# Performance work log

Hardware: AMD Instinct MI355X
Metric: run time of the kernel (lower is better)

The kernel has to match this reference:

```python
import jax, jax.numpy as jnp
import numpy as np

NUM_GRAPHS = 512  # number of segments (graphs) in the batch
N_NODES = 200000
HIDDEN = 256


def setup_inputs() -> dict:
    key = jax.random.key(0)
    ks = jax.random.split(key, 8)
    x = jax.random.normal(ks[0], (N_NODES, HIDDEN), dtype=jnp.float32)
    batch = jnp.sort(jax.random.randint(ks[1], (N_NODES,), 0, NUM_GRAPHS, dtype=jnp.int32))
    h4 = HIDDEN // 4
    w1 = jax.random.normal(ks[2], (HIDDEN, h4), dtype=jnp.float32) * (1.0 / np.sqrt(HIDDEN))
    b1 = jnp.zeros((h4,), dtype=jnp.float32)
    w2 = jax.random.normal(ks[3], (h4, 1), dtype=jnp.float32) * (1.0 / np.sqrt(h4))
    b2 = jnp.zeros((1,), dtype=jnp.float32)
    wp = jax.random.normal(ks[4], (3 * HIDDEN, HIDDEN), dtype=jnp.float32) * (1.0 / np.sqrt(3 * HIDDEN))
    bp = jnp.zeros((HIDDEN,), dtype=jnp.float32)
    gamma = jnp.ones((HIDDEN,), dtype=jnp.float32)
    beta = jnp.zeros((HIDDEN,), dtype=jnp.float32)
    return {"x": x, "batch": batch, "w1": w1, "b1": b1, "w2": w2, "b2": b2,
            "wp": wp, "bp": bp, "gamma": gamma, "beta": beta}


def reference(x, batch, w1, b1, w2, b2, wp, bp, gamma, beta):
    G = NUM_GRAPHS
    # --- global mean pool ---
    seg_sum = jax.ops.segment_sum(x, batch, num_segments=G)  # [G, H]
    counts = jax.ops.segment_sum(jnp.ones((x.shape[0],), x.dtype), batch, num_segments=G)
    z_mean = seg_sum / jnp.maximum(counts, 1.0)[:, None]
    # --- global max pool ---
    z_max = jax.ops.segment_max(x, batch, num_segments=G)
    z_max = jnp.where(jnp.isfinite(z_max), z_max, 0.0)  # guard empty segments
    # --- global attention pool (PyG GlobalAttention) ---
    gate = jnp.maximum(x @ w1 + b1, 0.0) @ w2 + b2  # [N, 1]
    g = gate[:, 0]
    g_max = jax.ops.segment_max(g, batch, num_segments=G)
    g_max = jnp.where(jnp.isfinite(g_max), g_max, 0.0)
    e = jnp.exp(g - g_max[batch])
    denom = jax.ops.segment_sum(e, batch, num_segments=G)
    w = e / jnp.maximum(denom, 1e-16)[batch]  # scatter-softmax weights [N]
    z_attn = jax.ops.segment_sum(w[:, None] * x, batch, num_segments=G)
    # --- concat + proj + layernorm ---
    z = jnp.concatenate([z_mean, z_max, z_attn], axis=-1)  # [G, 3H]
    y = z @ wp + bp  # [G, H]
    mu = jnp.mean(y, axis=-1, keepdims=True)
    var = jnp.mean(jnp.square(y - mu), axis=-1, keepdims=True)
    yhat = (y - mu) * jax.lax.rsqrt(var + 1e-5)
    return yhat * gamma + beta
```

## Files before the change

kernel.cpp:

```cpp
#include <hip/hip_runtime.h>
#include <math.h>

#define N_NODES 200000
#define NGRAPH  512
#define HID     256
#define NTILES  (N_NODES / 16)
#define NBLK    256
#define NWAVE   (NBLK * 4)
#define TPW     (NTILES / NWAVE)
#define TREM    (NTILES - NWAVE * TPW)

typedef __attribute__((ext_vector_type(8))) short s16x8;
typedef __attribute__((ext_vector_type(4))) float f32x4;

__device__ __forceinline__ unsigned int pack2_bf16_rne(float a, float b) {
  unsigned int ua = __float_as_uint(a), ub = __float_as_uint(b);
  unsigned int ra = (ua + 0x7fffu + ((ua >> 16) & 1u)) >> 16;
  unsigned int rb = (ub + 0x7fffu + ((ub >> 16) & 1u)) & 0xffff0000u;
  return ra | rb;
}
__device__ __forceinline__ int lower_bound_batch(const int* __restrict__ batch, int target) {
  int lo = 0, hi = N_NODES;
  while (lo < hi) { int mid = (lo + hi) >> 1; if (batch[mid] < target) lo = mid + 1; else hi = mid; }
  return lo;
}
__device__ __forceinline__ unsigned fkey(float f) {
  unsigned u = __float_as_uint(f);
  return (u >> 31) ? ~u : (u | 0x80000000u);
}

__global__ __launch_bounds__(256, 1) void fused_gate_pool(
    const float* __restrict__ x, const int* __restrict__ batch,
    const float* __restrict__ w1, const float* __restrict__ b1,
    const float* __restrict__ w2, const float* __restrict__ b2,
    float* __restrict__ gsum, unsigned* __restrict__ gmx,
    float* __restrict__ gat, float* __restrict__ gden)
{
  struct Buf { float xrow[16][256]; int bat[64]; };
  __shared__ __align__(16) Buf stg[4][2];

  const int tid = threadIdx.x;
  const int w = tid >> 6, lane = tid & 63, q = lane >> 4, c = lane & 15;
  const int gw = blockIdx.x * 4 + w;

  const int t0   = gw * TPW + (gw < TREM ? gw : TREM);
  const int tend = t0 + TPW + (gw < TREM ? 1 : 0);

  s16x8 bh[4][8];
#pragma unroll
  for (int nt = 0; nt < 4; ++nt) {
#pragma unroll
    for (int kt = 0; kt < 8; ++kt) {
      float f[8];
#pragma unroll
      for (int j = 0; j < 8; ++j)
        f[j] = w1[(size_t)(kt * 32 + q * 8 + j) * 64 + nt * 16 + c];
      union { s16x8 v; unsigned u[4]; } tmp;
      tmp.u[0] = pack2_bf16_rne(f[0], f[1]);
      tmp.u[1] = pack2_bf16_rne(f[2], f[3]);
      tmp.u[2] = pack2_bf16_rne(f[4], f[5]);
      tmp.u[3] = pack2_bf16_rne(f[6], f[7]);
      bh[nt][kt] = tmp.v;
    }
  }
  float b1v[4], w2v[4];
#pragma unroll
  for (int nt = 0; nt < 4; ++nt) { b1v[nt] = b1[nt * 16 + c]; w2v[nt] = w2[nt * 16 + c]; }
  const float b2v = b2[0];

  int soff[8];
#pragma unroll
  for (int s = 0; s < 8; ++s) soff[s] = (lane * 16) ^ (s << 4);
  const int csw = (c & 7) << 4;

  f32x4 sum = (f32x4){0.f, 0.f, 0.f, 0.f};
  f32x4 at  = (f32x4){0.f, 0.f, 0.f, 0.f};
  f32x4 mx  = (f32x4){-INFINITY, -INFINITY, -INFINITY, -INFINITY};
  float den = 0.f;
  int curseg = -1;

  auto STAGE = [&](int t, int b) {
    const char* rowbase = (const char*)x + (size_t)t * 16384;
#pragma unroll
    for (int r = 0; r < 16; ++r) {
      const void* gp = rowbase + r * 1024 + soff[r & 7];
      __builtin_amdgcn_global_load_lds(
          (const __attribute__((address_space(1))) void*)gp,
          (__attribute__((address_space(3))) void*)&stg[w][b].xrow[r][0],
          16, 0, 0);
    }
    const void* bp2 = (const void*)(batch + t * 16 + (lane & 15));
    __builtin_amdgcn_global_load_lds(
        (const __attribute__((address_space(1))) void*)bp2,
        (__attribute__((address_space(3))) void*)&stg[w][b].bat[0],
        4, 0, 0);
  };

  auto FLUSH = [&](int seg) {
    float* sp = gsum + (size_t)seg * 256 + lane * 4;
    float* ap = gat  + (size_t)seg * 256 + lane * 4;
    unsigned* mp = gmx + (size_t)seg * 256 + lane * 4;
#pragma unroll
    for (int j = 0; j < 4; ++j) {
      atomicAdd(&sp[j], sum[j]);
      atomicAdd(&ap[j], at[j]);
      atomicMax(&mp[j], fkey(mx[j]));
    }
    if (lane == 0) atomicAdd(&gden[seg], den);
  };

  STAGE(t0, 0);
  STAGE(t0 + 1, 1);

  for (int t = t0; t < tend; ++t) {
    const int b = (t - t0) & 1;
    if (t + 1 < tend) { asm volatile("s_waitcnt vmcnt(17)" ::: "memory"); }
    else              { asm volatile("s_waitcnt vmcnt(0)"  ::: "memory"); }
    __builtin_amdgcn_sched_barrier(0);

    const char* rb = (const char*)&stg[w][b].xrow[c][0];
    union { s16x8 v; unsigned u[4]; } ah[8];
#pragma unroll
    for (int kt = 0; kt < 8; ++kt) {
      const int base = kt * 128 + q * 32;
      float4 t0v = *(const float4*)(rb + ((base)      ^ csw));
      float4 t1v = *(const float4*)(rb + ((base + 16) ^ csw));
      ah[kt].u[0] = pack2_bf16_rne(t0v.x, t0v.y);
      ah[kt].u[1] = pack2_bf16_rne(t0v.z, t0v.w);
      ah[kt].u[2] = pack2_bf16_rne(t1v.x, t1v.y);
      ah[kt].u[3] = pack2_bf16_rne(t1v.z, t1v.w);
    }

    f32x4 acc[4];
#pragma unroll
    for (int nt = 0; nt < 4; ++nt) acc[nt] = (f32x4){0.f, 0.f, 0.f, 0.f};
#pragma unroll
    for (int kt = 0; kt < 8; ++kt) {
#pragma unroll
      for (int nt = 0; nt < 4; ++nt)
        acc[nt] = __builtin_amdgcn_mfma_f32_16x16x32_bf16(ah[kt].v, bh[nt][kt], acc[nt], 0, 0, 0);
    }

    float er[4];
#pragma unroll
    for (int r = 0; r < 4; ++r) {
      float sv = 0.f;
#pragma unroll
      for (int nt = 0; nt < 4; ++nt) {
        float h = acc[nt][r] + b1v[nt];
        h = h > 0.f ? h : 0.f;
        sv += h * w2v[nt];
      }
      sv += __shfl_xor(sv, 1, 64);
      sv += __shfl_xor(sv, 2, 64);
      sv += __shfl_xor(sv, 4, 64);
      sv += __shfl_xor(sv, 8, 64);
      er[r] = __expf(sv + b2v);
    }

#pragma unroll
    for (int i = 0; i < 16; ++i) {
      int sg = __builtin_amdgcn_readfirstlane(stg[w][b].bat[i]);
      if (sg != curseg) {
        if (curseg >= 0) FLUSH(curseg);
        sum = (f32x4){0.f, 0.f, 0.f, 0.f};
        at  = (f32x4){0.f, 0.f, 0.f, 0.f};
        mx  = (f32x4){-INFINITY, -INFINITY, -INFINITY, -INFINITY};
        den = 0.f;
        curseg = sg;
      }
      float ei = __shfl(er[i & 3], (i >> 2) << 4, 64);
      const float4 v = *(const float4*)((const char*)&stg[w][b].xrow[i][0] +
                                        ((lane * 16) ^ ((i & 7) << 4)));
      den += ei;
      sum[0] += v.x; sum[1] += v.y; sum[2] += v.z; sum[3] += v.w;
      mx[0] = fmaxf(mx[0], v.x); mx[1] = fmaxf(mx[1], v.y);
      mx[2] = fmaxf(mx[2], v.z); mx[3] = fmaxf(mx[3], v.w);
      at[0] = fmaf(ei, v.x, at[0]); at[1] = fmaf(ei, v.y, at[1]);
      at[2] = fmaf(ei, v.z, at[2]); at[3] = fmaf(ei, v.w, at[3]);
    }

    if (t + 2 < tend) STAGE(t + 2, b);
  }
  if (curseg >= 0) FLUSH(curseg);
}

__global__ __launch_bounds__(256) void head_ln(
    const float* __restrict__ gsum, const unsigned* __restrict__ gmx,
    const float* __restrict__ gat, const float* __restrict__ gden,
    const int* __restrict__ batch, const float* __restrict__ wp,
    const float* __restrict__ bp, const float* __restrict__ gam,
    const float* __restrict__ bet, float* __restrict__ out)
{
  const int g = blockIdx.x;
  const int tid = threadIdx.x;
  const int w = tid >> 6, lane = tid & 63;
  __shared__ int sb[2];
  __shared__ float z[768];
  __shared__ __align__(16) float part[4][256];
  __shared__ float red[256];

  if (tid < 2) sb[tid] = lower_bound_batch(batch, g + tid);
  __syncthreads();
  const float cnt = (float)(sb[1] - sb[0]);

  {
    const float s = gsum[(size_t)g * 256 + tid];
    const unsigned k = gmx[(size_t)g * 256 + tid];
    const unsigned u = (k & 0x80000000u) ? (k ^ 0x80000000u) : ~k;
    const float a = gat[(size_t)g * 256 + tid];
    const float den = gden[g];
    z[tid]       = (cnt > 0.f) ? s / cnt : 0.f;
    z[256 + tid] = (cnt > 0.f) ? __uint_as_float(u) : 0.f;
    z[512 + tid] = a / fmaxf(den, 1e-16f);
  }
  __syncthreads();

  f32x4 acc = (f32x4){0.f, 0.f, 0.f, 0.f};
  const float4* wp4 = (const float4*)wp;
  const int k0 = w * 192;
#pragma unroll 8
  for (int k = k0; k < k0 + 192; ++k) {
    float4 wv = wp4[(size_t)k * 64 + lane];
    float zk = z[k];
    acc[0] = fmaf(zk, wv.x, acc[0]);
    acc[1] = fmaf(zk, wv.y, acc[1]);
    acc[2] = fmaf(zk, wv.z, acc[2]);
    acc[3] = fmaf(zk, wv.w, acc[3]);
  }
  *(f32x4*)&part[w][lane * 4] = acc;
  __syncthreads();

  const int t = tid;
  float y = bp[t] + part[0][t] + part[1][t] + part[2][t] + part[3][t];

  red[t] = y;
  __syncthreads();
  for (int wd = 128; wd > 0; wd >>= 1) {
    if (t < wd) red[t] += red[t + wd];
    __syncthreads();
  }
  const float mu = red[0] * (1.f / 256.f);
  __syncthreads();
  float d = y - mu;
  red[t] = d * d;
  __syncthreads();
  for (int wd = 128; wd > 0; wd >>= 1) {
    if (t < wd) red[t] += red[t + wd];
    __syncthreads();
  }
  const float var = red[0] * (1.f / 256.f);
  const float is = rsqrtf(var + 1e-5f);
  out[(size_t)g * 256 + t] = fmaf(d * is, gam[t], bet[t]);
}

extern "C" void kernel_launch(void* const* d_in, const int* in_sizes, int n_in,
                              void* d_out, int out_size, void* d_ws, size_t ws_size,
                              hipStream_t stream) {
  const float* x   = (const float*)d_in[0];
  const int*   bat = (const int*)d_in[1];
  const float* w1  = (const float*)d_in[2];
  const float* b1  = (const float*)d_in[3];
  const float* w2  = (const float*)d_in[4];
  const float* b2  = (const float*)d_in[5];
  const float* wp  = (const float*)d_in[6];
  const float* bp  = (const float*)d_in[7];
  const float* gam = (const float*)d_in[8];
  const float* bet = (const float*)d_in[9];
  float* out = (float*)d_out;

  float* gsum   = (float*)d_ws;
  unsigned* gmx = (unsigned*)(gsum + (size_t)NGRAPH * 256);
  float* gat    = (float*)(gmx + (size_t)NGRAPH * 256);
  float* gden   = gat + (size_t)NGRAPH * 256;
  const size_t zbytes = ((size_t)NGRAPH * 256 * 3 + NGRAPH) * 4;

  hipMemsetAsync(d_ws, 0, zbytes, stream);
  hipLaunchKernelGGL(fused_gate_pool, dim3(NBLK), dim3(256), 0, stream,
                     x, bat, w1, b1, w2, b2, gsum, gmx, gat, gden);
  hipLaunchKernelGGL(head_ln, dim3(NGRAPH), dim3(256), 0, stream,
                     gsum, gmx, gat, gden, bat, wp, bp, gam, bet, out);
}
```

Before: 339.7 us.

## Replace LDS-direct double buffering with register prefetch and two blocks per CU

Drops the global_load_lds double-buffered staging and instead prefetches the next 16-row tile into registers, writing it into a single swizzled LDS buffer each iteration. It doubles the grid to 512 blocks with launch bounds allowing 2 blocks per CU, relying on occupancy rather than explicit vmcnt pipelining to hide latency. It also reads segment ids from global memory and adds a fast path when a whole tile belongs to one segment. This costs extra VGPRs for the prefetch and puts scalar batch loads on the critical path. With one LDS buffer, the wave's own reads and writes must stay ordered.

Result: slower. 462.9 us (+36.2%).

```diff
diff --git a/kernel.cpp b/kernel.cpp
--- a/kernel.cpp
+++ b/kernel.cpp
@@ -5,7 +5,7 @@
 #define NGRAPH  512
 #define HID     256
 #define NTILES  (N_NODES / 16)
-#define NBLK    256
+#define NBLK    512
 #define NWAVE   (NBLK * 4)
 #define TPW     (NTILES / NWAVE)
 #define TREM    (NTILES - NWAVE * TPW)
@@ -29,15 +29,15 @@
   return (u >> 31) ? ~u : (u | 0x80000000u);
 }
 
-__global__ __launch_bounds__(256, 1) void fused_gate_pool(
+__global__ __launch_bounds__(256, 2) void fused_gate_pool(
     const float* __restrict__ x, const int* __restrict__ batch,
     const float* __restrict__ w1, const float* __restrict__ b1,
     const float* __restrict__ w2, const float* __restrict__ b2,
     float* __restrict__ gsum, unsigned* __restrict__ gmx,
     float* __restrict__ gat, float* __restrict__ gden)
 {
-  struct Buf { float xrow[16][256]; int bat[64]; };
-  __shared__ __align__(16) Buf stg[4][2];
+  struct Buf { float xrow[16][256]; };
+  __shared__ __align__(16) Buf stg[4];
 
   const int tid = threadIdx.x;
   const int w = tid >> 6, lane = tid & 63, q = lane >> 4, c = lane & 15;
@@ -68,9 +68,6 @@
   for (int nt = 0; nt < 4; ++nt) { b1v[nt] = b1[nt * 16 + c]; w2v[nt] = w2[nt * 16 + c]; }
   const float b2v = b2[0];
 
-  int soff[8];
-#pragma unroll
-  for (int s = 0; s < 8; ++s) soff[s] = (lane * 16) ^ (s << 4);
   const int csw = (c & 7) << 4;
 
   f32x4 sum = (f32x4){0.f, 0.f, 0.f, 0.f};
@@ -79,23 +76,18 @@
   float den = 0.f;
   int curseg = -1;
 
-  auto STAGE = [&](int t, int b) {
-    const char* rowbase = (const char*)x + (size_t)t * 16384;
-#pragma unroll
-    for (int r = 0; r < 16; ++r) {
-      const void* gp = rowbase + r * 1024 + soff[r & 7];
-      __builtin_amdgcn_global_load_lds(
-          (const __attribute__((address_space(1))) void*)gp,
-          (__attribute__((address_space(3))) void*)&stg[w][b].xrow[r][0],
-          16, 0, 0);
-    }
-    const void* bp2 = (const void*)(batch + t * 16 + (lane & 15));
-    __builtin_amdgcn_global_load_lds(
-        (const __attribute__((address_space(1))) void*)bp2,
-        (__attribute__((address_space(3))) void*)&stg[w][b].bat[0],
-        4, 0, 0);
-  };
-
+  float4 pf[16];
+  auto LOADR = [&](int t) {
+    const float* rowbase = x + (size_t)t * 4096 + lane * 4;
+#pragma unroll
+    for (int r = 0; r < 16; ++r)
+      pf[r] = *(const float4*)(rowbase + r * 256);
+  };
+  auto WRITE = [&]() {
+#pragma unroll
+    for (int r = 0; r < 16; ++r)
+      *(float4*)((char*)&stg[w].xrow[r][0] + ((lane * 16) ^ ((r & 7) << 4))) = pf[r];
+  };
   auto FLUSH = [&](int seg) {
     float* sp = gsum + (size_t)seg * 256 + lane * 4;
     float* ap = gat  + (size_t)seg * 256 + lane * 4;
@@ -108,17 +100,20 @@
     }
     if (lane == 0) atomicAdd(&gden[seg], den);
   };
-
-  STAGE(t0, 0);
-  STAGE(t0 + 1, 1);
+  auto RESET = [&]() {
+    sum = (f32x4){0.f, 0.f, 0.f, 0.f};
+    at  = (f32x4){0.f, 0.f, 0.f, 0.f};
+    mx  = (f32x4){-INFINITY, -INFINITY, -INFINITY, -INFINITY};
+    den = 0.f;
+  };
+
+  LOADR(t0);
 
   for (int t = t0; t < tend; ++t) {
-    const int b = (t - t0) & 1;
-    if (t + 1 < tend) { asm volatile("s_waitcnt vmcnt(17)" ::: "memory"); }
-    else              { asm volatile("s_waitcnt vmcnt(0)"  ::: "memory"); }
-    __builtin_amdgcn_sched_barrier(0);
-
-    const char* rb = (const char*)&stg[w][b].xrow[c][0];
+    WRITE();
+    if (t + 1 < tend) LOADR(t + 1);
+
+    const char* rb = (const char*)&stg[w].xrow[c][0];
     union { s16x8 v; unsigned u[4]; } ah[8];
 #pragma unroll
     for (int kt = 0; kt < 8; ++kt) {
@@ -157,30 +152,49 @@
       sv += __shfl_xor(sv, 8, 64);
       er[r] = __expf(sv + b2v);
     }
-
-#pragma unroll
-    for (int i = 0; i < 16; ++i) {
-      int sg = __builtin_amdgcn_readfirstlane(stg[w][b].bat[i]);
-      if (sg != curseg) {
+    float ei[16];
+#pragma unroll
+    for (int i = 0; i < 16; ++i) ei[i] = __shfl(er[i & 3], (i >> 2) << 4, 64);
+
+    const int r0t = t << 4;
+    const int sg0  = batch[r0t];
+    const int sg15 = batch[r0t + 15];
+    if (sg0 == sg15) {
+      if (sg0 != curseg) {
         if (curseg >= 0) FLUSH(curseg);
-        sum = (f32x4){0.f, 0.f, 0.f, 0.f};
-        at  = (f32x4){0.f, 0.f, 0.f, 0.f};
-        mx  = (f32x4){-INFINITY, -INFINITY, -INFINITY, -INFINITY};
-        den = 0.f;
-        curseg = sg;
-      }
-      float ei = __shfl(er[i & 3], (i >> 2) << 4, 64);
-      const float4 v = *(const float4*)((const char*)&stg[w][b].xrow[i][0] +
-                                        ((lane * 16) ^ ((i & 7) << 4)));
-      den += ei;
-      sum[0] += v.x; sum[1] += v.y; sum[2] += v.z; sum[3] += v.w;
-      mx[0] = fmaxf(mx[0], v.x); mx[1] = fmaxf(mx[1], v.y);
-      mx[2] = fmaxf(mx[2], v.z); mx[3] = fmaxf(mx[3], v.w);
-      at[0] = fmaf(ei, v.x, at[0]); at[1] = fmaf(ei, v.y, at[1]);
-      at[2] = fmaf(ei, v.z, at[2]); at[3] = fmaf(ei, v.w, at[3]);
-    }
-
-    if (t + 2 < tend) STAGE(t + 2, b);
+        RESET();
+        curseg = sg0;
+      }
+#pragma unroll
+      for (int i = 0; i < 16; ++i) {
+        const float4 v = *(const float4*)((const char*)&stg[w].xrow[i][0] +
+                                          ((lane * 16) ^ ((i & 7) << 4)));
+        den += ei[i];
+        sum[0] += v.x; sum[1] += v.y; sum[2] += v.z; sum[3] += v.w;
+        mx[0] = fmaxf(mx[0], v.x); mx[1] = fmaxf(mx[1], v.y);
+        mx[2] = fmaxf(mx[2], v.z); mx[3] = fmaxf(mx[3], v.w);
+        at[0] = fmaf(ei[i], v.x, at[0]); at[1] = fmaf(ei[i], v.y, at[1]);
+        at[2] = fmaf(ei[i], v.z, at[2]); at[3] = fmaf(ei[i], v.w, at[3]);
+      }
+    } else {
+#pragma unroll
+      for (int i = 0; i < 16; ++i) {
+        const int sg = batch[r0t + i];
+        if (sg != curseg) {
+          if (curseg >= 0) FLUSH(curseg);
+          RESET();
+          curseg = sg;
+        }
+        const float4 v = *(const float4*)((const char*)&stg[w].xrow[i][0] +
+                                          ((lane * 16) ^ ((i & 7) << 4)));
+        den += ei[i];
+        sum[0] += v.x; sum[1] += v.y; sum[2] += v.z; sum[3] += v.w;
+        mx[0] = fmaxf(mx[0], v.x); mx[1] = fmaxf(mx[1], v.y);
+        mx[2] = fmaxf(mx[2], v.z); mx[3] = fmaxf(mx[3], v.w);
+        at[0] = fmaf(ei[i], v.x, at[0]); at[1] = fmaf(ei[i], v.y, at[1]);
+        at[2] = fmaf(ei[i], v.z, at[2]); at[3] = fmaf(ei[i], v.w, at[3]);
+      }
+    }
   }
   if (curseg >= 0) FLUSH(curseg);
 }
```
